# Performance work log

Measured on AMD Instinct MI355X. Metric: run time of the kernel, lower is better.

The kernel has to match this reference:

```python
import jax, jax.numpy as jnp
import numpy as np

DIM = 768
HEADS = 12
FRAMES = 16
T = FRAMES // 2          # temporal length per stream = 8
N = 196                  # spatial patch tokens (14x14)
B = 16                   # batch
SCALE = (DIM // HEADS) ** -0.5


def setup_inputs() -> dict:
    key = jax.random.key(0)
    ks = jax.random.split(key, 10)
    return {
        "s_x": jax.random.normal(ks[0], (N + 1, B * T, DIM), jnp.float32),
        "t_x": jax.random.normal(ks[1], (B, T * N, DIM), jnp.float32),
        "clip_time_pos": SCALE * jax.random.normal(ks[2], (T, DIM), jnp.float32),
        "vmae_time_pos": SCALE * jax.random.normal(ks[3], (T, DIM), jnp.float32),
        "Wq": jax.random.normal(ks[4], (DIM, DIM), jnp.float32) * 0.02,
        "q_bias": jnp.zeros((DIM,), jnp.float32),
        "Wkv": jax.random.normal(ks[5], (2 * DIM, DIM), jnp.float32) * 0.02,
        "kv_bias": jnp.zeros((2 * DIM,), jnp.float32),
        "Wproj": jax.random.normal(ks[6], (DIM, DIM), jnp.float32) * 0.02,
        "proj_bias": jnp.zeros((DIM,), jnp.float32),
    }


def reference(s_x, t_x, clip_time_pos, vmae_time_pos,
              Wq, q_bias, Wkv, kv_bias, Wproj, proj_bias):
    b = t_x.shape[0]
    t = s_x.shape[1] // b            # = FRAMES // 2
    n = s_x.shape[0] - 1             # spatial tokens (CLS excluded)
    d = s_x.shape[-1]
    h = HEADS
    hd = d // h
    scale = hd ** -0.5

    s_cls = s_x[0]                                   # [b*t, d]
    # 'n (b t) d -> (b n) t d'
    s_pat = s_x[1:].reshape(n, b, t, d).transpose(1, 0, 2, 3).reshape(b * n, t, d)
    s_pat = s_pat + clip_time_pos                    # [(b n), t, d]
    # 'b (t n) d -> (b n) t d'
    tx = t_x.reshape(b, t, n, d).transpose(0, 2, 1, 3).reshape(b * n, t, d)
    tx = tx + vmae_time_pos

    # projections (bias added manually as in F.linear with explicit bias)
    q = (s_pat @ Wq.T + q_bias).reshape(b * n, t, h, hd).transpose(0, 2, 1, 3)  # [bn,h,t,hd]
    kv = (tx @ Wkv.T + kv_bias).reshape(b * n, t, 2, h, hd)                      # e outermost in (e h d)
    k = kv[:, :, 0].transpose(0, 2, 1, 3)            # [bn,h,t,hd]
    v = kv[:, :, 1].transpose(0, 2, 1, 3)

    attn = jax.nn.softmax(jnp.einsum('bhqd,bhkd->bhqk', q * scale, k), axis=-1)
    out = jnp.einsum('bhqk,bhkd->bhqd', attn, v)     # [bn,h,t,hd]
    out = out.transpose(0, 2, 1, 3).reshape(b * n, t, d)
    out = out @ Wproj.T + proj_bias
    # '(b n) t d -> n (b t) d'
    out = out.reshape(b, n, t, d).transpose(1, 0, 2, 3).reshape(n, b * t, d)
    return jnp.concatenate([s_cls[None], out], axis=0)
```

## Files before the change

kernel.cpp:

```cpp
#include <hip/hip_runtime.h>
#include <stdint.h>

#define DIM   768
#define NTOK  196
#define TT    8
#define MROWS 25088
#define HEADS 12
#define NKT   12

typedef __bf16 bf16x8 __attribute__((ext_vector_type(8)));
typedef float  f32x4  __attribute__((ext_vector_type(4)));
typedef unsigned short u16x4 __attribute__((ext_vector_type(4)));
typedef unsigned short u16x8 __attribute__((ext_vector_type(8)));

typedef __attribute__((address_space(1))) const void GAS;
typedef __attribute__((address_space(3))) void LAS;

__device__ inline unsigned short f2bf(float f) {
  uint32_t u = __builtin_bit_cast(uint32_t, f);
  u += 0x7FFFu + ((u >> 16) & 1u);
  return (unsigned short)(u >> 16);
}
__device__ inline float bf2f(unsigned short s) {
  uint32_t u = ((uint32_t)s) << 16;
  return __builtin_bit_cast(float, u);
}
__device__ inline void gl_lds16(const unsigned short* g, unsigned short* l) {
  __builtin_amdgcn_global_load_lds((GAS*)g, (LAS*)l, 16, 0, 0);
}
__device__ inline int xcd_swz(int orig, int nwg) {
  int xcd = orig & 7, loc = orig >> 3;
  int q = nwg >> 3, r = nwg & 7;
  int base = (xcd < r) ? xcd * (q + 1) : r * (q + 1) + (xcd - r) * q;
  return base + loc;
}

#define WAITV(n) asm volatile("s_waitcnt vmcnt(" #n ")" ::: "memory")

__global__ void wprep_kernel(const float* __restrict__ wq,
                             const float* __restrict__ wkv,
                             const float* __restrict__ wproj,
                             unsigned short* __restrict__ out) {
  int idx4 = blockIdx.x * blockDim.x + threadIdx.x;
  const int total4 = 2359296 / 4;
  if (idx4 >= total4) return;
  int e = idx4 * 4;
  const float* src; int off;
  if (e < 589824)        { src = wq;    off = e; }
  else if (e < 1769472)  { src = wkv;   off = e - 589824; }
  else                   { src = wproj; off = e - 1769472; }
  f32x4 v = *reinterpret_cast<const f32x4*>(&src[off]);
  u16x4 o;
  o[0] = f2bf(v[0]); o[1] = f2bf(v[1]); o[2] = f2bf(v[2]); o[3] = f2bf(v[3]);
  *reinterpret_cast<u16x4*>(&out[e]) = o;
}

__global__ void cls_kernel(const float* __restrict__ sx, float* __restrict__ out) {
  int i4 = blockIdx.x * blockDim.x + threadIdx.x;
  if (i4 < (128 * 768) / 4)
    reinterpret_cast<f32x4*>(out)[i4] = reinterpret_cast<const f32x4*>(sx)[i4];
}

template<int MODE>
__global__ __launch_bounds__(256)
void aprep_kernel(const float* __restrict__ src, const float* __restrict__ timepos,
                  unsigned short* __restrict__ dst) {
  int idx = blockIdx.x * blockDim.x + threadIdx.x;
  const int total = MROWS * (DIM / 8);
  if (idx >= total) return;
  int m  = idx / 96;
  int c8 = (idx - m * 96) * 8;
  int bn = m >> 3, t = m & 7;
  int b  = bn / NTOK, n = bn - b * NTOK;
  int srow = (MODE == 0) ? ((1 + n) * 128 + b * 8 + t)
                         : (b * (TT * NTOK) + t * NTOK + n);
  const float* sp = &src[srow * DIM + c8];
  const float* pp = &timepos[t * DIM + c8];
  f32x4 a0 = reinterpret_cast<const f32x4*>(sp)[0];
  f32x4 a1 = reinterpret_cast<const f32x4*>(sp)[1];
  f32x4 p0 = reinterpret_cast<const f32x4*>(pp)[0];
  f32x4 p1 = reinterpret_cast<const f32x4*>(pp)[1];
  a0 += p0; a1 += p1;
  u16x8 o;
  o[0] = f2bf(a0[0]); o[1] = f2bf(a0[1]); o[2] = f2bf(a0[2]); o[3] = f2bf(a0[3]);
  o[4] = f2bf(a1[0]); o[5] = f2bf(a1[1]); o[6] = f2bf(a1[2]); o[7] = f2bf(a1[3]);
  *reinterpret_cast<u16x8*>(&dst[m * DIM + c8]) = o;
}

template<int MODE>
__global__ __launch_bounds__(512)
void gemm8(const unsigned short* __restrict__ As,
           const unsigned short* __restrict__ At,
           const unsigned short* __restrict__ W0,
           const unsigned short* __restrict__ W1,
           const float* __restrict__ b0,
           const float* __restrict__ b1,
           unsigned short* __restrict__ out0,
           unsigned short* __restrict__ out1,
           float* __restrict__ fout,
           int bid0) {
  __shared__ unsigned short SB[3 * 24576];

  const int tid  = threadIdx.x;
  const int lane = tid & 63;
  const int w    = tid >> 6;
  const int wm   = w >> 2;
  const int wn   = w & 3;

  int bid = xcd_swz(blockIdx.x, gridDim.x) + bid0;

  const unsigned short *Ag, *Wg;
  const float* bias;
  unsigned short* ob = nullptr;
  int rt, ct, Ncols;
  float scale = 1.0f;
  if (MODE == 0) {
    if (bid < 588) { rt = bid / 6;  ct = bid % 6;  Ag = As; Wg = W0; bias = b0; ob = out0; Ncols = 768;  scale = 0.125f; }
    else { int b2 = bid - 588; rt = b2 / 12; ct = b2 % 12; Ag = At; Wg = W1; bias = b1; ob = out1; Ncols = 1536; }
  } else {
    rt = bid / 6; ct = bid % 6; Ag = As; Wg = W0; bias = b0; Ncols = 768;
  }
  const int m0 = rt * 256;
  const int n0 = ct * 128;

  auto stageA = [&](int kt) {
    const int kb = kt * 64;
    unsigned short* dst = &SB[(kt % 3) * 24576];
    #pragma unroll
    for (int rnd = 0; rnd < 4; ++rnd) {
      int s    = rnd * 8 + w;
      int srow = s * 8 + (lane >> 3);
      int scol = ((lane & 7) * 8) ^ ((srow & 7) << 3);
      gl_lds16(&Ag[(size_t)(m0 + srow) * 768 + kb + scol], dst + s * 512);
    }
  };
  auto stageB = [&](int kt) {
    const int kb = kt * 64;
    unsigned short* dst = &SB[(kt % 3) * 24576 + 16384];
    #pragma unroll
    for (int rnd = 0; rnd < 2; ++rnd) {
      int s    = rnd * 8 + w;
      int srow = s * 8 + (lane >> 3);
      int scol = ((lane & 7) * 8) ^ ((srow & 7) << 3);
      gl_lds16(&Wg[(size_t)(n0 + srow) * 768 + kb + scol], dst + s * 512);
    }
  };

  f32x4 acc[8][2] = {};

  stageA(0); stageB(0);
  stageA(1); stageB(1);

  for (int kt = 0; kt < NKT; ++kt) {
    __builtin_amdgcn_sched_barrier(0);
    if (kt < NKT - 1) { WAITV(6); } else { WAITV(0); }
    __builtin_amdgcn_s_barrier();
    asm volatile("" ::: "memory");

    const unsigned short* Ab = &SB[(kt % 3) * 24576];
    const unsigned short* Bb = Ab + 16384;
    const bool st = (kt + 2) < NKT;

    if (st) stageA(kt + 2);
    __builtin_amdgcn_sched_barrier(0);

    #pragma unroll
    for (int ks = 0; ks < 2; ++ks) {
      bf16x8 af[8], bfv[2];
      const int kc = ks * 32 + (lane >> 4) * 8;
      #pragma unroll
      for (int fm = 0; fm < 8; ++fm) {
        int r = wm * 128 + fm * 16 + (lane & 15);
        af[fm] = *reinterpret_cast<const bf16x8*>(&Ab[r * 64 + (kc ^ ((r & 7) << 3))]);
      }
      #pragma unroll
      for (int fn = 0; fn < 2; ++fn) {
        int r = wn * 32 + fn * 16 + (lane & 15);
        bfv[fn] = *reinterpret_cast<const bf16x8*>(&Bb[r * 64 + (kc ^ ((r & 7) << 3))]);
      }
      __builtin_amdgcn_s_setprio(1);
      #pragma unroll
      for (int fm = 0; fm < 8; ++fm)
        #pragma unroll
        for (int fn = 0; fn < 2; ++fn)
          acc[fm][fn] = __builtin_amdgcn_mfma_f32_16x16x32_bf16(af[fm], bfv[fn], acc[fm][fn], 0, 0, 0);
      __builtin_amdgcn_s_setprio(0);
      if (ks == 0 && st) stageB(kt + 2);
      __builtin_amdgcn_sched_barrier(0);
    }
  }

  #pragma unroll
  for (int fm = 0; fm < 8; ++fm) {
    #pragma unroll
    for (int fn = 0; fn < 2; ++fn) {
      int col = n0 + wn * 32 + fn * 16 + (lane & 15);
      float bsv = bias[col];
      #pragma unroll
      for (int i = 0; i < 4; ++i) {
        int row = m0 + wm * 128 + fm * 16 + (lane >> 4) * 4 + i;
        float v = acc[fm][fn][i] + bsv;
        if (MODE == 0) {
          v *= scale;
          ob[(size_t)row * Ncols + col] = f2bf(v);
        } else {
          int bn = row >> 3, t = row & 7;
          int b  = bn / NTOK, n = bn - b * NTOK;
          fout[((1 + n) * 128 + b * 8 + t) * DIM + col] = v;
        }
      }
    }
  }
}

__global__ __launch_bounds__(256)
void attn_kernel(const unsigned short* __restrict__ qb,
                 const unsigned short* __restrict__ kvb,
                 unsigned short* __restrict__ ob) {
  __shared__ __align__(16) float lds[4][3][8][68];
  const int tid  = threadIdx.x;
  const int lane = tid & 63;
  const int w    = tid >> 6;
  const int wid  = blockIdx.x * 4 + w;
  const int bn   = wid / HEADS;
  const int h    = wid - bn * HEADS;

  const int t  = lane >> 3;
  const int d0 = (lane & 7) * 8;
  const int qoff = (bn * 8 + t) * DIM + h * 64 + d0;
  const int koff = (bn * 8 + t) * (2 * DIM) + h * 64 + d0;

  u16x8 q8 = *reinterpret_cast<const u16x8*>(&qb[qoff]);
  u16x8 k8 = *reinterpret_cast<const u16x8*>(&kvb[koff]);
  u16x8 v8 = *reinterpret_cast<const u16x8*>(&kvb[koff + DIM]);
  f32x4 qa, qc, ka, kc, va, vc;
  #pragma unroll
  for (int e = 0; e < 4; ++e) {
    qa[e] = bf2f(q8[e]); qc[e] = bf2f(q8[e + 4]);
    ka[e] = bf2f(k8[e]); kc[e] = bf2f(k8[e + 4]);
    va[e] = bf2f(v8[e]); vc[e] = bf2f(v8[e + 4]);
  }
  *reinterpret_cast<f32x4*>(&lds[w][0][t][d0])     = qa;
  *reinterpret_cast<f32x4*>(&lds[w][0][t][d0 + 4]) = qc;
  *reinterpret_cast<f32x4*>(&lds[w][1][t][d0])     = ka;
  *reinterpret_cast<f32x4*>(&lds[w][1][t][d0 + 4]) = kc;
  *reinterpret_cast<f32x4*>(&lds[w][2][t][d0])     = va;
  *reinterpret_cast<f32x4*>(&lds[w][2][t][d0 + 4]) = vc;
  __syncthreads();

  const int i = lane >> 3, j = lane & 7;
  const f32x4* qi = reinterpret_cast<const f32x4*>(&lds[w][0][i][0]);
  const f32x4* kj = reinterpret_cast<const f32x4*>(&lds[w][1][j][0]);
  float s = 0.f;
  #pragma unroll
  for (int c = 0; c < 16; ++c) {
    f32x4 a = qi[c], b = kj[c];
    s += a[0] * b[0] + a[1] * b[1] + a[2] * b[2] + a[3] * b[3];
  }
  float m = s;
  m = fmaxf(m, __shfl_xor(m, 1));
  m = fmaxf(m, __shfl_xor(m, 2));
  m = fmaxf(m, __shfl_xor(m, 4));
  float e = __expf(s - m);
  float sum = e;
  sum += __shfl_xor(sum, 1);
  sum += __shfl_xor(sum, 2);
  sum += __shfl_xor(sum, 4);
  float p = e / sum;

  float o[8] = {};
  #pragma unroll
  for (int jj = 0; jj < 8; ++jj) {
    float pj = __shfl(p, (lane & 56) | jj);
    const f32x4* vj = reinterpret_cast<const f32x4*>(&lds[w][2][jj][d0]);
    f32x4 v0 = vj[0], v1 = vj[1];
    o[0] += pj * v0[0]; o[1] += pj * v0[1]; o[2] += pj * v0[2]; o[3] += pj * v0[3];
    o[4] += pj * v1[0]; o[5] += pj * v1[1]; o[6] += pj * v1[2]; o[7] += pj * v1[3];
  }
  u16x8 os;
  #pragma unroll
  for (int e2 = 0; e2 < 8; ++e2) os[e2] = f2bf(o[e2]);
  *reinterpret_cast<u16x8*>(&ob[qoff]) = os;
}

extern "C" void kernel_launch(void* const* d_in, const int* in_sizes, int n_in,
                              void* d_out, int out_size, void* d_ws, size_t ws_size,
                              hipStream_t stream) {
  const float* s_x       = (const float*)d_in[0];
  const float* t_x       = (const float*)d_in[1];
  const float* clip_pos  = (const float*)d_in[2];
  const float* vmae_pos  = (const float*)d_in[3];
  const float* Wq        = (const float*)d_in[4];
  const float* q_bias    = (const float*)d_in[5];
  const float* Wkv       = (const float*)d_in[6];
  const float* kv_bias   = (const float*)d_in[7];
  const float* Wproj     = (const float*)d_in[8];
  const float* proj_bias = (const float*)d_in[9];
  float* out = (float*)d_out;

  char* ws = (char*)d_ws;
  unsigned short* w_bf = (unsigned short*)ws;
  const size_t ABUF = 38535168, KVB = 77070336, WB = 4718592;
  const bool merged = ws_size >= (WB + 3 * ABUF + KVB);

  const unsigned short* wq_bf = w_bf;
  const unsigned short* wkv_bf = w_bf + 589824;
  const unsigned short* wpj_bf = w_bf + 1769472;

  const int prep_blocks = (MROWS * 96 + 255) / 256;

  wprep_kernel<<<dim3((589824 + 255) / 256), dim3(256), 0, stream>>>(Wq, Wkv, Wproj, w_bf);
  cls_kernel<<<dim3(96), dim3(256), 0, stream>>>(s_x, out);

  if (merged) {
    unsigned short* As    = (unsigned short*)(ws + WB);
    unsigned short* At    = (unsigned short*)(ws + WB + ABUF);
    unsigned short* q_bf  = (unsigned short*)(ws + WB + 2 * ABUF);
    unsigned short* kv_bf = (unsigned short*)(ws + WB + 3 * ABUF);
    aprep_kernel<0><<<dim3(prep_blocks), dim3(256), 0, stream>>>(s_x, clip_pos, As);
    aprep_kernel<1><<<dim3(prep_blocks), dim3(256), 0, stream>>>(t_x, vmae_pos, At);
    gemm8<0><<<dim3(1764), dim3(512), 0, stream>>>(As, At, wq_bf, wkv_bf, q_bias, kv_bias,
                                                   q_bf, kv_bf, nullptr, 0);
    attn_kernel<<<dim3(9408), dim3(256), 0, stream>>>(q_bf, kv_bf, As);
    gemm8<1><<<dim3(588), dim3(512), 0, stream>>>(As, nullptr, wpj_bf, nullptr, proj_bias,
                                                  nullptr, nullptr, nullptr, out, 0);
  } else {
    unsigned short* buf1  = (unsigned short*)(ws + WB);
    unsigned short* q_bf  = (unsigned short*)(ws + WB + ABUF);
    unsigned short* kv_bf = (unsigned short*)(ws + WB + 2 * ABUF);
    aprep_kernel<0><<<dim3(prep_blocks), dim3(256), 0, stream>>>(s_x, clip_pos, buf1);
    gemm8<0><<<dim3(588), dim3(512), 0, stream>>>(buf1, buf1, wq_bf, wkv_bf, q_bias, kv_bias,
                                                  q_bf, kv_bf, nullptr, 0);
    aprep_kernel<1><<<dim3(prep_blocks), dim3(256), 0, stream>>>(t_x, vmae_pos, buf1);
    gemm8<0><<<dim3(1176), dim3(512), 0, stream>>>(buf1, buf1, wq_bf, wkv_bf, q_bias, kv_bias,
                                                   q_bf, kv_bf, nullptr, 588);
    attn_kernel<<<dim3(9408), dim3(256), 0, stream>>>(q_bf, kv_bf, buf1);
    gemm8<1><<<dim3(588), dim3(512), 0, stream>>>(buf1, nullptr, wpj_bf, nullptr, proj_bias,
                                                  nullptr, nullptr, nullptr, out, 0);
  }
}
```

Baseline: 212.4 us.

## Fuse prep kernels and replace pipelined 256x128 GEMM with simple 128x128 tiles

Merges the weight-cast, CLS-copy and both activation-prep kernels into one launch. The triple-buffered, 512-thread GEMM with 256x128 tiles is replaced by a single-buffered 256-thread kernel using 128x128 tiles and launch bounds that allow four blocks per CU. This relies on occupancy rather than software pipelining to hide load latency. The trade-off is that the explicit load/compute overlap is dropped, and each tile now has a lower arithmetic intensity.

```diff
diff --git a/kernel.cpp b/kernel.cpp
--- a/kernel.cpp
+++ b/kernel.cpp
@@ -35,172 +35,147 @@
   return base + loc;
 }
 
-#define WAITV(n) asm volatile("s_waitcnt vmcnt(" #n ")" ::: "memory")
-
-__global__ void wprep_kernel(const float* __restrict__ wq,
-                             const float* __restrict__ wkv,
-                             const float* __restrict__ wproj,
-                             unsigned short* __restrict__ out) {
-  int idx4 = blockIdx.x * blockDim.x + threadIdx.x;
-  const int total4 = 2359296 / 4;
-  if (idx4 >= total4) return;
-  int e = idx4 * 4;
-  const float* src; int off;
-  if (e < 589824)        { src = wq;    off = e; }
-  else if (e < 1769472)  { src = wkv;   off = e - 589824; }
-  else                   { src = wproj; off = e - 1769472; }
-  f32x4 v = *reinterpret_cast<const f32x4*>(&src[off]);
-  u16x4 o;
-  o[0] = f2bf(v[0]); o[1] = f2bf(v[1]); o[2] = f2bf(v[2]); o[3] = f2bf(v[3]);
-  *reinterpret_cast<u16x4*>(&out[e]) = o;
-}
-
-__global__ void cls_kernel(const float* __restrict__ sx, float* __restrict__ out) {
-  int i4 = blockIdx.x * blockDim.x + threadIdx.x;
-  if (i4 < (128 * 768) / 4)
-    reinterpret_cast<f32x4*>(out)[i4] = reinterpret_cast<const f32x4*>(sx)[i4];
-}
-
-template<int MODE>
 __global__ __launch_bounds__(256)
-void aprep_kernel(const float* __restrict__ src, const float* __restrict__ timepos,
-                  unsigned short* __restrict__ dst) {
-  int idx = blockIdx.x * blockDim.x + threadIdx.x;
-  const int total = MROWS * (DIM / 8);
-  if (idx >= total) return;
-  int m  = idx / 96;
-  int c8 = (idx - m * 96) * 8;
-  int bn = m >> 3, t = m & 7;
-  int b  = bn / NTOK, n = bn - b * NTOK;
-  int srow = (MODE == 0) ? ((1 + n) * 128 + b * 8 + t)
-                         : (b * (TT * NTOK) + t * NTOK + n);
-  const float* sp = &src[srow * DIM + c8];
-  const float* pp = &timepos[t * DIM + c8];
-  f32x4 a0 = reinterpret_cast<const f32x4*>(sp)[0];
-  f32x4 a1 = reinterpret_cast<const f32x4*>(sp)[1];
-  f32x4 p0 = reinterpret_cast<const f32x4*>(pp)[0];
-  f32x4 p1 = reinterpret_cast<const f32x4*>(pp)[1];
-  a0 += p0; a1 += p1;
-  u16x8 o;
-  o[0] = f2bf(a0[0]); o[1] = f2bf(a0[1]); o[2] = f2bf(a0[2]); o[3] = f2bf(a0[3]);
-  o[4] = f2bf(a1[0]); o[5] = f2bf(a1[1]); o[6] = f2bf(a1[2]); o[7] = f2bf(a1[3]);
-  *reinterpret_cast<u16x8*>(&dst[m * DIM + c8]) = o;
-}
-
-template<int MODE>
-__global__ __launch_bounds__(512)
-void gemm8(const unsigned short* __restrict__ As,
-           const unsigned short* __restrict__ At,
-           const unsigned short* __restrict__ W0,
-           const unsigned short* __restrict__ W1,
-           const float* __restrict__ b0,
-           const float* __restrict__ b1,
-           unsigned short* __restrict__ out0,
-           unsigned short* __restrict__ out1,
-           float* __restrict__ fout,
-           int bid0) {
-  __shared__ unsigned short SB[3 * 24576];
+void prep_all(const float* __restrict__ wq, const float* __restrict__ wkv,
+              const float* __restrict__ wproj, unsigned short* __restrict__ w_bf,
+              const float* __restrict__ s_x, const float* __restrict__ t_x,
+              const float* __restrict__ clip, const float* __restrict__ vmae,
+              unsigned short* __restrict__ As, unsigned short* __restrict__ At,
+              float* __restrict__ cls_out, int bbase) {
+  const int bx = blockIdx.x + bbase;
+  if (bx < 2304) {
+    int idx4 = bx * 256 + threadIdx.x;
+    int e = idx4 * 4;
+    const float* src; int off;
+    if (e < 589824)        { src = wq;    off = e; }
+    else if (e < 1769472)  { src = wkv;   off = e - 589824; }
+    else                   { src = wproj; off = e - 1769472; }
+    f32x4 v = *reinterpret_cast<const f32x4*>(&src[off]);
+    u16x4 o;
+    o[0] = f2bf(v[0]); o[1] = f2bf(v[1]); o[2] = f2bf(v[2]); o[3] = f2bf(v[3]);
+    *reinterpret_cast<u16x4*>(&w_bf[e]) = o;
+  } else if (bx < 2400) {
+    int i4 = (bx - 2304) * 256 + threadIdx.x;
+    reinterpret_cast<f32x4*>(cls_out)[i4] = reinterpret_cast<const f32x4*>(s_x)[i4];
+  } else {
+    const bool isS = bx < 11808;
+    int idx = (bx - (isS ? 2400 : 11808)) * 256 + threadIdx.x;
+    int m  = idx / 96;
+    int c8 = (idx - m * 96) * 8;
+    int bn = m >> 3, t = m & 7;
+    int b  = bn / NTOK, n = bn - b * NTOK;
+    const float* src; const float* tp; unsigned short* dst; int srow;
+    if (isS) { srow = (1 + n) * 128 + b * 8 + t;      src = s_x; tp = clip; dst = As; }
+    else     { srow = b * (TT * NTOK) + t * NTOK + n; src = t_x; tp = vmae; dst = At; }
+    const float* sp = &src[srow * DIM + c8];
+    const float* pp = &tp[t * DIM + c8];
+    f32x4 a0 = reinterpret_cast<const f32x4*>(sp)[0];
+    f32x4 a1 = reinterpret_cast<const f32x4*>(sp)[1];
+    f32x4 p0 = reinterpret_cast<const f32x4*>(pp)[0];
+    f32x4 p1 = reinterpret_cast<const f32x4*>(pp)[1];
+    a0 += p0; a1 += p1;
+    u16x8 o;
+    o[0] = f2bf(a0[0]); o[1] = f2bf(a0[1]); o[2] = f2bf(a0[2]); o[3] = f2bf(a0[3]);
+    o[4] = f2bf(a1[0]); o[5] = f2bf(a1[1]); o[6] = f2bf(a1[2]); o[7] = f2bf(a1[3]);
+    *reinterpret_cast<u16x8*>(&dst[m * DIM + c8]) = o;
+  }
+}
+
+template<int PROJ>
+__global__ __launch_bounds__(256, 4)
+void gemm97(const unsigned short* __restrict__ As,
+            const unsigned short* __restrict__ At,
+            const unsigned short* __restrict__ W0,
+            const unsigned short* __restrict__ W1,
+            const float* __restrict__ b0,
+            const float* __restrict__ b1,
+            unsigned short* __restrict__ out0,
+            unsigned short* __restrict__ out1,
+            float* __restrict__ fout, int bid0) {
+  __shared__ unsigned short SA[8192];
+  __shared__ unsigned short SBB[8192];
 
   const int tid  = threadIdx.x;
   const int lane = tid & 63;
   const int w    = tid >> 6;
-  const int wm   = w >> 2;
-  const int wn   = w & 3;
-
-  int bid = xcd_swz(blockIdx.x, gridDim.x) + bid0;
+  const int wm   = w >> 1;
+  const int wn   = w & 1;
+
+  const int bid = xcd_swz(blockIdx.x, gridDim.x) + bid0;
 
   const unsigned short *Ag, *Wg;
   const float* bias;
   unsigned short* ob = nullptr;
-  int rt, ct, Ncols;
+  int rt, ct, Ncols = 768;
   float scale = 1.0f;
-  if (MODE == 0) {
-    if (bid < 588) { rt = bid / 6;  ct = bid % 6;  Ag = As; Wg = W0; bias = b0; ob = out0; Ncols = 768;  scale = 0.125f; }
-    else { int b2 = bid - 588; rt = b2 / 12; ct = b2 % 12; Ag = At; Wg = W1; bias = b1; ob = out1; Ncols = 1536; }
+  if (PROJ == 0) {
+    if (bid < 1176) { rt = bid / 6;  ct = bid % 6;  Ag = As; Wg = W0; bias = b0; ob = out0; Ncols = 768;  scale = 0.125f; }
+    else { int b2 = bid - 1176; rt = b2 / 12; ct = b2 % 12; Ag = At; Wg = W1; bias = b1; ob = out1; Ncols = 1536; }
   } else {
-    rt = bid / 6; ct = bid % 6; Ag = As; Wg = W0; bias = b0; Ncols = 768;
-  }
-  const int m0 = rt * 256;
+    rt = bid / 6; ct = bid % 6; Ag = As; Wg = W0; bias = b0;
+  }
+  const int m0 = rt * 128;
   const int n0 = ct * 128;
 
-  auto stageA = [&](int kt) {
-    const int kb = kt * 64;
-    unsigned short* dst = &SB[(kt % 3) * 24576];
+  auto stA = [&](int kt) {
     #pragma unroll
     for (int rnd = 0; rnd < 4; ++rnd) {
-      int s    = rnd * 8 + w;
-      int srow = s * 8 + (lane >> 3);
+      int srow = rnd * 32 + w * 8 + (lane >> 3);
       int scol = ((lane & 7) * 8) ^ ((srow & 7) << 3);
-      gl_lds16(&Ag[(size_t)(m0 + srow) * 768 + kb + scol], dst + s * 512);
+      gl_lds16(&Ag[(size_t)(m0 + srow) * 768 + kt * 64 + scol], &SA[(rnd * 4 + w) * 512]);
     }
   };
-  auto stageB = [&](int kt) {
-    const int kb = kt * 64;
-    unsigned short* dst = &SB[(kt % 3) * 24576 + 16384];
+  auto stB = [&](int kt) {
     #pragma unroll
-    for (int rnd = 0; rnd < 2; ++rnd) {
-      int s    = rnd * 8 + w;
-      int srow = s * 8 + (lane >> 3);
+    for (int rnd = 0; rnd < 4; ++rnd) {
+      int srow = rnd * 32 + w * 8 + (lane >> 3);
       int scol = ((lane & 7) * 8) ^ ((srow & 7) << 3);
-      gl_lds16(&Wg[(size_t)(n0 + srow) * 768 + kb + scol], dst + s * 512);
+      gl_lds16(&Wg[(size_t)(n0 + srow) * 768 + kt * 64 + scol], &SBB[(rnd * 4 + w) * 512]);
     }
   };
 
-  f32x4 acc[8][2] = {};
-
-  stageA(0); stageB(0);
-  stageA(1); stageB(1);
+  f32x4 acc[4][4] = {};
 
   for (int kt = 0; kt < NKT; ++kt) {
-    __builtin_amdgcn_sched_barrier(0);
-    if (kt < NKT - 1) { WAITV(6); } else { WAITV(0); }
-    __builtin_amdgcn_s_barrier();
-    asm volatile("" ::: "memory");
-
-    const unsigned short* Ab = &SB[(kt % 3) * 24576];
-    const unsigned short* Bb = Ab + 16384;
-    const bool st = (kt + 2) < NKT;
-
-    if (st) stageA(kt + 2);
-    __builtin_amdgcn_sched_barrier(0);
+    stA(kt); stB(kt);
+    __syncthreads();
 
     #pragma unroll
     for (int ks = 0; ks < 2; ++ks) {
-      bf16x8 af[8], bfv[2];
+      bf16x8 af[4], bfv[4];
       const int kc = ks * 32 + (lane >> 4) * 8;
       #pragma unroll
-      for (int fm = 0; fm < 8; ++fm) {
-        int r = wm * 128 + fm * 16 + (lane & 15);
-        af[fm] = *reinterpret_cast<const bf16x8*>(&Ab[r * 64 + (kc ^ ((r & 7) << 3))]);
+      for (int fm = 0; fm < 4; ++fm) {
+        int r = wm * 64 + fm * 16 + (lane & 15);
+        af[fm] = *reinterpret_cast<const bf16x8*>(&SA[r * 64 + (kc ^ ((r & 7) << 3))]);
       }
       #pragma unroll
-      for (int fn = 0; fn < 2; ++fn) {
-        int r = wn * 32 + fn * 16 + (lane & 15);
-        bfv[fn] = *reinterpret_cast<const bf16x8*>(&Bb[r * 64 + (kc ^ ((r & 7) << 3))]);
+      for (int fn = 0; fn < 4; ++fn) {
+        int r = wn * 64 + fn * 16 + (lane & 15);
+        bfv[fn] = *reinterpret_cast<const bf16x8*>(&SBB[r * 64 + (kc ^ ((r & 7) << 3))]);
       }
       __builtin_amdgcn_s_setprio(1);
       #pragma unroll
-      for (int fm = 0; fm < 8; ++fm)
+      for (int fm = 0; fm < 4; ++fm)
         #pragma unroll
-        for (int fn = 0; fn < 2; ++fn)
+        for (int fn = 0; fn < 4; ++fn)
           acc[fm][fn] = __builtin_amdgcn_mfma_f32_16x16x32_bf16(af[fm], bfv[fn], acc[fm][fn], 0, 0, 0);
       __builtin_amdgcn_s_setprio(0);
-      if (ks == 0 && st) stageB(kt + 2);
-      __builtin_amdgcn_sched_barrier(0);
     }
-  }
-
-  #pragma unroll
-  for (int fm = 0; fm < 8; ++fm) {
+    __syncthreads();
+  }
+
+  #pragma unroll
+  for (int fm = 0; fm < 4; ++fm) {
     #pragma unroll
-    for (int fn = 0; fn < 2; ++fn) {
-      int col = n0 + wn * 32 + fn * 16 + (lane & 15);
+    for (int fn = 0; fn < 4; ++fn) {
+      int col = n0 + wn * 64 + fn * 16 + (lane & 15);
       float bsv = bias[col];
       #pragma unroll
       for (int i = 0; i < 4; ++i) {
-        int row = m0 + wm * 128 + fm * 16 + (lane >> 4) * 4 + i;
+        int row = m0 + wm * 64 + fm * 16 + (lane >> 4) * 4 + i;
         float v = acc[fm][fn][i] + bsv;
-        if (MODE == 0) {
+        if (PROJ == 0) {
           v *= scale;
           ob[(size_t)row * Ncols + col] = f2bf(v);
         } else {
@@ -303,39 +278,36 @@
   const size_t ABUF = 38535168, KVB = 77070336, WB = 4718592;
   const bool merged = ws_size >= (WB + 3 * ABUF + KVB);
 
-  const unsigned short* wq_bf = w_bf;
+  const unsigned short* wq_bf  = w_bf;
   const unsigned short* wkv_bf = w_bf + 589824;
   const unsigned short* wpj_bf = w_bf + 1769472;
-
-  const int prep_blocks = (MROWS * 96 + 255) / 256;
-
-  wprep_kernel<<<dim3((589824 + 255) / 256), dim3(256), 0, stream>>>(Wq, Wkv, Wproj, w_bf);
-  cls_kernel<<<dim3(96), dim3(256), 0, stream>>>(s_x, out);
 
   if (merged) {
     unsigned short* As    = (unsigned short*)(ws + WB);
     unsigned short* At    = (unsigned short*)(ws + WB + ABUF);
     unsigned short* q_bf  = (unsigned short*)(ws + WB + 2 * ABUF);
     unsigned short* kv_bf = (unsigned short*)(ws + WB + 3 * ABUF);
-    aprep_kernel<0><<<dim3(prep_blocks), dim3(256), 0, stream>>>(s_x, clip_pos, As);
-    aprep_kernel<1><<<dim3(prep_blocks), dim3(256), 0, stream>>>(t_x, vmae_pos, At);
-    gemm8<0><<<dim3(1764), dim3(512), 0, stream>>>(As, At, wq_bf, wkv_bf, q_bias, kv_bias,
-                                                   q_bf, kv_bf, nullptr, 0);
+    prep_all<<<dim3(21216), dim3(256), 0, stream>>>(
+        Wq, Wkv, Wproj, w_bf, s_x, t_x, clip_pos, vmae_pos, As, At, out, 0);
+    gemm97<0><<<dim3(3528), dim3(256), 0, stream>>>(
+        As, At, wq_bf, wkv_bf, q_bias, kv_bias, q_bf, kv_bf, nullptr, 0);
     attn_kernel<<<dim3(9408), dim3(256), 0, stream>>>(q_bf, kv_bf, As);
-    gemm8<1><<<dim3(588), dim3(512), 0, stream>>>(As, nullptr, wpj_bf, nullptr, proj_bias,
-                                                  nullptr, nullptr, nullptr, out, 0);
+    gemm97<1><<<dim3(1176), dim3(256), 0, stream>>>(
+        As, nullptr, wpj_bf, nullptr, proj_bias, nullptr, nullptr, nullptr, out, 0);
   } else {
     unsigned short* buf1  = (unsigned short*)(ws + WB);
     unsigned short* q_bf  = (unsigned short*)(ws + WB + ABUF);
     unsigned short* kv_bf = (unsigned short*)(ws + WB + 2 * ABUF);
-    aprep_kernel<0><<<dim3(prep_blocks), dim3(256), 0, stream>>>(s_x, clip_pos, buf1);
-    gemm8<0><<<dim3(588), dim3(512), 0, stream>>>(buf1, buf1, wq_bf, wkv_bf, q_bias, kv_bias,
-                                                  q_bf, kv_bf, nullptr, 0);
-    aprep_kernel<1><<<dim3(prep_blocks), dim3(256), 0, stream>>>(t_x, vmae_pos, buf1);
-    gemm8<0><<<dim3(1176), dim3(512), 0, stream>>>(buf1, buf1, wq_bf, wkv_bf, q_bias, kv_bias,
-                                                   q_bf, kv_bf, nullptr, 588);
+    prep_all<<<dim3(11808), dim3(256), 0, stream>>>(
+        Wq, Wkv, Wproj, w_bf, s_x, t_x, clip_pos, vmae_pos, buf1, buf1, out, 0);
+    gemm97<0><<<dim3(1176), dim3(256), 0, stream>>>(
+        buf1, buf1, wq_bf, wkv_bf, q_bias, kv_bias, q_bf, kv_bf, nullptr, 0);
+    prep_all<<<dim3(9408), dim3(256), 0, stream>>>(
+        Wq, Wkv, Wproj, w_bf, s_x, t_x, clip_pos, vmae_pos, buf1, buf1, out, 11808);
+    gemm97<0><<<dim3(2352), dim3(256), 0, stream>>>(
+        buf1, buf1, wq_bf, wkv_bf, q_bias, kv_bias, q_bf, kv_bf, nullptr, 1176);
     attn_kernel<<<dim3(9408), dim3(256), 0, stream>>>(q_bf, kv_bf, buf1);
-    gemm8<1><<<dim3(588), dim3(512), 0, stream>>>(buf1, nullptr, wpj_bf, nullptr, proj_bias,
-                                                  nullptr, nullptr, nullptr, out, 0);
-  }
-}
+    gemm97<1><<<dim3(1176), dim3(256), 0, stream>>>(
+        buf1, nullptr, wpj_bf, nullptr, proj_bias, nullptr, nullptr, nullptr, out, 0);
+  }
+}
```

After: 201.1 us. 1.06x faster.
